# Kernel tuning notes

Measured on AMD Instinct MI355X. Metric: run time of the kernel, lower is better.

The kernel has to match this reference:

```python
import jax, jax.numpy as jnp
import numpy as np

B, H, W, C = 32, 512, 512, 3


def setup_inputs() -> dict:
    key = jax.random.key(0)
    k1, k2, k3 = jax.random.split(key, 3)
    images = jax.random.normal(k1, (B, H, W, C), dtype=jnp.float32)
    # focal lengths in pixels, positive and well-conditioned
    focal = 400.0 + 200.0 * jax.random.uniform(k2, (B, 2), dtype=jnp.float32)
    # quaternion ~ identity rotation + small noise (stddev=0.01), q0 mean 1
    q = jnp.array([1.0, 0.0, 0.0, 0.0], jnp.float32) + 0.01 * jax.random.normal(k3, (4,), dtype=jnp.float32)
    return {"images": images, "focal": focal, "q": q}


def _quaternion_to_R(q):
    # matches tf_quaternion_to_R: normalize so sum(q^2)=2, then outer product
    q = q * jnp.sqrt(2.0 / jnp.sum(q * q))
    Q = q[:, None] * q[None, :]  # [4,4], Q[i,j] = q_i q_j
    return jnp.array([
        [1.0 - Q[2, 2] - Q[3, 3], Q[1, 2] - Q[3, 0], Q[1, 3] + Q[2, 0]],
        [Q[1, 2] + Q[3, 0], 1.0 - Q[1, 1] - Q[3, 3], Q[2, 3] - Q[1, 0]],
        [Q[1, 3] - Q[2, 0], Q[2, 3] + Q[1, 0], 1.0 - Q[1, 1] - Q[2, 2]],
    ])


def _forward(images, focal, q):
    R = _quaternion_to_R(q)  # [3,3]
    d = jnp.concatenate([focal, jnp.ones((focal.shape[0], 1), focal.dtype)], axis=1)  # [B,3]
    # H = K @ R @ inv(K) with K = diag(d):  H[b,i,j] = d[b,i] * R[i,j] / d[b,j]
    Hm = R[None, :, :] * d[:, :, None] / d[:, None, :]  # [B,3,3]

    origin_x = jnp.float32(W / 2)
    origin_y = jnp.float32(H / 2)
    xs = jnp.arange(W, dtype=jnp.float32) - origin_x  # [W]
    ys = jnp.arange(H, dtype=jnp.float32) - origin_y  # [H]
    x, y = jnp.meshgrid(xs, ys)  # [H,W] each
    ps = jnp.stack([x.ravel(), y.ravel(), jnp.ones(H * W, jnp.float32)], axis=0)  # [3,N]

    ps_w = jnp.einsum('bij,jn->bin', Hm, ps)  # [B,3,N]
    x_w = (ps_w[:, 0, :] / ps_w[:, 2, :]).reshape(-1, H, W) + origin_x  # [B,H,W]
    y_w = (ps_w[:, 1, :] / ps_w[:, 2, :]).reshape(-1, H, W) + origin_y  # [B,H,W]

    # bilinear resampler (tf.contrib.resampler): zero outside image bounds
    x0 = jnp.floor(x_w)
    y0 = jnp.floor(y_w)
    wx = x_w - x0
    wy = y_w - y0
    x0i = x0.astype(jnp.int32)
    y0i = y0.astype(jnp.int32)

    b = jnp.arange(images.shape[0])[:, None, None]

    def corner(yi, xi, w):
        valid = (xi >= 0) & (xi <= W - 1) & (yi >= 0) & (yi <= H - 1)
        g = images[b, jnp.clip(yi, 0, H - 1), jnp.clip(xi, 0, W - 1)]  # [B,H,W,C]
        return g * (w * valid.astype(images.dtype))[..., None]

    out = (corner(y0i, x0i, (1.0 - wx) * (1.0 - wy))
           + corner(y0i, x0i + 1, wx * (1.0 - wy))
           + corner(y0i + 1, x0i, (1.0 - wx) * wy)
           + corner(y0i + 1, x0i + 1, wx * wy))
    return out


def reference(images, focal, q):
    return _forward(images, focal, q)
```

## Files before the change

### kernel.cpp

```cpp
#include <hip/hip_runtime.h>
#include <hip/hip_bf16.h>


#define IMG_H 512
#define IMG_W 512
#define IMG_C 3
#define NB    32

typedef float f32x4u __attribute__((ext_vector_type(4), aligned(4)));
typedef float f32x2u __attribute__((ext_vector_type(2), aligned(4)));

__global__ __launch_bounds__(256) void warp_kernel(
    const float* __restrict__ images,
    const float* __restrict__ focal,
    const float* __restrict__ q,
    float* __restrict__ out)
{
    const unsigned bid  = blockIdx.x;
    const unsigned xcd  = bid & 7u;
    const unsigned slot = bid >> 3;
    const unsigned virt = xcd * 2048u + slot;
    const int b = (int)(virt >> 9);
    const int y = (int)(virt & 511u);

    const int tid = threadIdx.x;

    float q0 = q[0], q1 = q[1], q2 = q[2], q3 = q[3];
    {
        float s = sqrtf(2.0f / (q0*q0 + q1*q1 + q2*q2 + q3*q3));
        q0 *= s; q1 *= s; q2 *= s; q3 *= s;
    }
    const float R00 = 1.0f - q2*q2 - q3*q3;
    const float R01 = q1*q2 - q3*q0;
    const float R02 = q1*q3 + q2*q0;
    const float R10 = q1*q2 + q3*q0;
    const float R11 = 1.0f - q1*q1 - q3*q3;
    const float R12 = q2*q3 - q1*q0;
    const float R20 = q1*q3 - q2*q0;
    const float R21 = q2*q3 + q1*q0;
    const float R22 = 1.0f - q1*q1 - q2*q2;
    const float d0 = focal[b*2 + 0];
    const float d1 = focal[b*2 + 1];

    const float h0 = (R00*d0)/d0;
    const float h1 = (R01*d0)/d1;
    const float h2 = (R02*d0);
    const float h3 = (R10*d1)/d0;
    const float h4 = (R11*d1)/d1;
    const float h5 = (R12*d1);
    const float h6 = R20/d0;
    const float h7 = R21/d1;
    const float h8 = R22;

    const float ys = (float)y - 256.0f;
    const float r1 = h1*ys + h2;
    const float r4 = h4*ys + h5;
    const float r7 = h7*ys + h8;

    const float* __restrict__ img_b = images + (unsigned)b * (IMG_H * IMG_W * IMG_C);

    #define SAMPLE(PX, A0, A1, A2) do {                                        \
        const float xs = (float)(PX) - 256.0f;                                 \
        float p0 = fmaf(h0, xs, r1);                                           \
        float p1 = fmaf(h3, xs, r4);                                           \
        float p2 = fmaf(h6, xs, r7);                                           \
        float rp2 = __builtin_amdgcn_rcpf(p2);                                 \
        float xw = fmaf(p0, rp2, 256.0f);                                      \
        float yw = fmaf(p1, rp2, 256.0f);                                      \
        float x0f = floorf(xw), y0f = floorf(yw);                              \
        float wx = xw - x0f,   wy = yw - y0f;                                  \
        int x0 = (int)x0f, y0i = (int)y0f;                                     \
        bool interior = (x0 >= 0) & (y0i >= 0) &                               \
                        (x0 < IMG_W-1) & (y0i < IMG_H-1);                      \
        if (__all(interior)) {                                                 \
             \
            const float* bpA = img_b + ((unsigned)y0i * IMG_W + (unsigned)x0) * 3u; \
            const float* bpB = bpA + IMG_W * 3u;                               \
            f32x4u vA0 = *reinterpret_cast<const f32x4u*>(bpA);                \
            f32x2u vA1 = *reinterpret_cast<const f32x2u*>(bpA + 4);            \
            f32x4u vB0 = *reinterpret_cast<const f32x4u*>(bpB);                \
            f32x2u vB1 = *reinterpret_cast<const f32x2u*>(bpB + 4);            \
            float w00 = (1.0f - wx) * (1.0f - wy);                             \
            float w01 = wx * (1.0f - wy);                                      \
            float w10 = (1.0f - wx) * wy;                                      \
            float w11 = wx * wy;                                               \
            A0 = vA0.x*w00 + vA0.w*w01 + vB0.x*w10 + vB0.w*w11;                \
            A1 = vA0.y*w00 + vA1.x*w01 + vB0.y*w10 + vB1.x*w11;                \
            A2 = vA0.z*w00 + vA1.y*w01 + vB0.z*w10 + vB1.y*w11;                \
        } else {                                                               \
                          \
            int x1 = x0 + 1, y1i = y0i + 1;                                    \
            bool vx0 = (x0 >= 0) & (x0 <= IMG_W-1);                            \
            bool vx1 = (x1 >= 0) & (x1 <= IMG_W-1);                            \
            bool vy0 = (y0i >= 0) & (y0i <= IMG_H-1);                          \
            bool vy1 = (y1i >= 0) & (y1i <= IMG_H-1);                          \
            unsigned xc0 = (unsigned)min(max(x0, 0), IMG_W-1);                 \
            unsigned xc1 = (unsigned)min(max(x1, 0), IMG_W-1);                 \
            unsigned yc0 = (unsigned)min(max(y0i, 0), IMG_H-1);                \
            unsigned yc1 = (unsigned)min(max(y1i, 0), IMG_H-1);                \
            const float* p00 = img_b + (yc0 * IMG_W + xc0) * IMG_C;            \
            const float* p01 = img_b + (yc0 * IMG_W + xc1) * IMG_C;            \
            const float* p10 = img_b + (yc1 * IMG_W + xc0) * IMG_C;            \
            const float* p11 = img_b + (yc1 * IMG_W + xc1) * IMG_C;            \
            float a00 = p00[0], a01 = p00[1], a02 = p00[2];                    \
            float b00 = p01[0], b01 = p01[1], b02 = p01[2];                    \
            float c00 = p10[0], c01 = p10[1], c02 = p10[2];                    \
            float d00 = p11[0], d01 = p11[1], d02 = p11[2];                    \
            float w00 = (vx0 & vy0) ? (1.0f - wx) * (1.0f - wy) : 0.0f;        \
            float w01 = (vx1 & vy0) ? wx * (1.0f - wy)          : 0.0f;        \
            float w10 = (vx0 & vy1) ? (1.0f - wx) * wy          : 0.0f;        \
            float w11 = (vx1 & vy1) ? wx * wy                   : 0.0f;        \
            A0 = a00*w00 + b00*w01 + c00*w10 + d00*w11;                        \
            A1 = a01*w00 + b01*w01 + c01*w10 + d01*w11;                        \
            A2 = a02*w00 + b02*w01 + c02*w10 + d02*w11;                        \
        }                                                                      \
    } while (0)

    const int px = tid * 2;
    float o0a, o1a, o2a, o0b, o1b, o2b;
    SAMPLE(px,     o0a, o1a, o2a);
    SAMPLE(px + 1, o0b, o1b, o2b);
    #undef SAMPLE

    float* outp = out + ((unsigned)(b * IMG_H + y)) * (IMG_W * IMG_C) + (unsigned)px * 3u;
    f32x4u s0; s0.x = o0a; s0.y = o1a; s0.z = o2a; s0.w = o0b;
    f32x2u s1; s1.x = o1b; s1.y = o2b;
    __builtin_nontemporal_store(s0, reinterpret_cast<f32x4u*>(outp));
    __builtin_nontemporal_store(s1, reinterpret_cast<f32x2u*>(outp + 4));
}

extern "C" void kernel_launch(void* const* d_in, const int* in_sizes, int n_in,
                              void* d_out, int out_size, void* d_ws, size_t ws_size,
                              hipStream_t stream) {
    const float* images = (const float*)d_in[0];
    const float* focal  = (const float*)d_in[1];
    const float* q      = (const float*)d_in[2];
    float* out = (float*)d_out;

    dim3 grid(16384);
    dim3 block(256);
    warp_kernel<<<grid, block, 0, stream>>>(images, focal, q, out);
}
```

Measured before the change: 38.92 us.

## Process eight rows per block with LDS-staged coalesced output stores

Each block now handles eight consecutive output rows instead of one, and the grid shrinks accordingly so per-block setup (quaternion, homography) is amortized. Each thread samples strided pixels tid and tid+256, and the results are staged in a double-buffered shared-memory row so global stores are aligned 16-byte coalesced vectors. This adds a __syncthreads per row and LDS traffic, and the strided pixel assignment changes the gather access pattern relative to the previous adjacent-pair scheme.

```diff
diff --git a/kernel.cpp b/kernel.cpp
--- a/kernel.cpp
+++ b/kernel.cpp
@@ -7,6 +7,7 @@
 #define IMG_C 3
 #define NB    32
 
+typedef float f32x4  __attribute__((ext_vector_type(4)));
 typedef float f32x4u __attribute__((ext_vector_type(4), aligned(4)));
 typedef float f32x2u __attribute__((ext_vector_type(2), aligned(4)));
 
@@ -19,11 +20,13 @@
     const unsigned bid  = blockIdx.x;
     const unsigned xcd  = bid & 7u;
     const unsigned slot = bid >> 3;
-    const unsigned virt = xcd * 2048u + slot;
-    const int b = (int)(virt >> 9);
-    const int y = (int)(virt & 511u);
+    const unsigned virt = xcd * 256u + slot;
+    const int b  = (int)(virt >> 6);
+    const int yg = (int)(virt & 63u) * 8;
 
     const int tid = threadIdx.x;
+
+    __shared__ float s_out[2][IMG_W * IMG_C];
 
     float q0 = q[0], q1 = q[1], q2 = q[2], q3 = q[3];
     {
@@ -52,18 +55,13 @@
     const float h7 = R21/d1;
     const float h8 = R22;
 
-    const float ys = (float)y - 256.0f;
-    const float r1 = h1*ys + h2;
-    const float r4 = h4*ys + h5;
-    const float r7 = h7*ys + h8;
-
     const float* __restrict__ img_b = images + (unsigned)b * (IMG_H * IMG_W * IMG_C);
 
-    #define SAMPLE(PX, A0, A1, A2) do {                                        \
+    #define SAMPLE(PX, R1, R4, R7, A0, A1, A2) do {                            \
         const float xs = (float)(PX) - 256.0f;                                 \
-        float p0 = fmaf(h0, xs, r1);                                           \
-        float p1 = fmaf(h3, xs, r4);                                           \
-        float p2 = fmaf(h6, xs, r7);                                           \
+        float p0 = fmaf(h0, xs, R1);                                           \
+        float p1 = fmaf(h3, xs, R4);                                           \
+        float p2 = fmaf(h6, xs, R7);                                           \
         float rp2 = __builtin_amdgcn_rcpf(p2);                                 \
         float xw = fmaf(p0, rp2, 256.0f);                                      \
         float yw = fmaf(p1, rp2, 256.0f);                                      \
@@ -116,17 +114,37 @@
         }                                                                      \
     } while (0)
 
-    const int px = tid * 2;
-    float o0a, o1a, o2a, o0b, o1b, o2b;
-    SAMPLE(px,     o0a, o1a, o2a);
-    SAMPLE(px + 1, o0b, o1b, o2b);
+    #pragma unroll 2
+    for (int i = 0; i < 8; ++i) {
+        const int y = yg + i;
+        const float ys = (float)y - 256.0f;
+        const float r1 = fmaf(h1, ys, h2);
+        const float r4 = fmaf(h4, ys, h5);
+        const float r7 = fmaf(h7, ys, h8);
+
+        float o0a, o1a, o2a, o0b, o1b, o2b;
+        SAMPLE(tid,       r1, r4, r7, o0a, o1a, o2a);
+        SAMPLE(tid + 256, r1, r4, r7, o0b, o1b, o2b);
+
+        float* buf = s_out[i & 1];
+        buf[tid*3 + 0] = o0a;
+        buf[tid*3 + 1] = o1a;
+        buf[tid*3 + 2] = o2a;
+        buf[(tid + 256)*3 + 0] = o0b;
+        buf[(tid + 256)*3 + 1] = o1b;
+        buf[(tid + 256)*3 + 2] = o2b;
+        __syncthreads();
+
+        f32x4* outp = reinterpret_cast<f32x4*>(
+            out + ((unsigned)(b * IMG_H + y)) * (IMG_W * IMG_C));
+        f32x4 v0 = *reinterpret_cast<const f32x4*>(&buf[tid * 4]);
+        __builtin_nontemporal_store(v0, &outp[tid]);
+        if (tid < 128) {
+            f32x4 v1 = *reinterpret_cast<const f32x4*>(&buf[(256 + tid) * 4]);
+            __builtin_nontemporal_store(v1, &outp[256 + tid]);
+        }
+    }
     #undef SAMPLE
-
-    float* outp = out + ((unsigned)(b * IMG_H + y)) * (IMG_W * IMG_C) + (unsigned)px * 3u;
-    f32x4u s0; s0.x = o0a; s0.y = o1a; s0.z = o2a; s0.w = o0b;
-    f32x2u s1; s1.x = o1b; s1.y = o2b;
-    __builtin_nontemporal_store(s0, reinterpret_cast<f32x4u*>(outp));
-    __builtin_nontemporal_store(s1, reinterpret_cast<f32x2u*>(outp + 4));
 }
 
 extern "C" void kernel_launch(void* const* d_in, const int* in_sizes, int n_in,
@@ -137,7 +155,7 @@
     const float* q      = (const float*)d_in[2];
     float* out = (float*)d_out;
 
-    dim3 grid(16384);
+    dim3 grid(2048);
     dim3 block(256);
     warp_kernel<<<grid, block, 0, stream>>>(images, focal, q, out);
 }
```

New measurement: 39.42 us. Within noise of the previous version (+1.3%).

## Share gather loads between adjacent pixels and stage output through LDS

Applied to the files above, without the earlier changes.

When both pixels of a thread fall in the same source row and their x-offsets differ by 0 or 1, a single set of wider loads from the two source rows serves both bilinear samples. This replaces two separate gathers per pixel. Results are written to shared memory first and then stored as aligned 16-byte vectors, so the global writes are fully coalesced instead of unaligned 4+2-float stores. The cost is a block-wide barrier, 6KB of LDS per block and extra select logic for the paired path.

```diff
diff --git a/kernel.cpp b/kernel.cpp
--- a/kernel.cpp
+++ b/kernel.cpp
@@ -7,8 +7,8 @@
 #define IMG_C 3
 #define NB    32
 
+typedef float f32x4  __attribute__((ext_vector_type(4)));
 typedef float f32x4u __attribute__((ext_vector_type(4), aligned(4)));
-typedef float f32x2u __attribute__((ext_vector_type(2), aligned(4)));
 
 __global__ __launch_bounds__(256) void warp_kernel(
     const float* __restrict__ images,
@@ -24,6 +24,8 @@
     const int y = (int)(virt & 511u);
 
     const int tid = threadIdx.x;
+
+    __shared__ float s_out[IMG_W * IMG_C];
 
     float q0 = q[0], q1 = q[1], q2 = q[2], q3 = q[3];
     {
@@ -59,44 +61,88 @@
 
     const float* __restrict__ img_b = images + (unsigned)b * (IMG_H * IMG_W * IMG_C);
 
-    #define SAMPLE(PX, A0, A1, A2) do {                                        \
-        const float xs = (float)(PX) - 256.0f;                                 \
-        float p0 = fmaf(h0, xs, r1);                                           \
-        float p1 = fmaf(h3, xs, r4);                                           \
-        float p2 = fmaf(h6, xs, r7);                                           \
-        float rp2 = __builtin_amdgcn_rcpf(p2);                                 \
-        float xw = fmaf(p0, rp2, 256.0f);                                      \
-        float yw = fmaf(p1, rp2, 256.0f);                                      \
-        float x0f = floorf(xw), y0f = floorf(yw);                              \
-        float wx = xw - x0f,   wy = yw - y0f;                                  \
-        int x0 = (int)x0f, y0i = (int)y0f;                                     \
-        bool interior = (x0 >= 0) & (y0i >= 0) &                               \
-                        (x0 < IMG_W-1) & (y0i < IMG_H-1);                      \
-        if (__all(interior)) {                                                 \
-             \
-            const float* bpA = img_b + ((unsigned)y0i * IMG_W + (unsigned)x0) * 3u; \
-            const float* bpB = bpA + IMG_W * 3u;                               \
-            f32x4u vA0 = *reinterpret_cast<const f32x4u*>(bpA);                \
-            f32x2u vA1 = *reinterpret_cast<const f32x2u*>(bpA + 4);            \
-            f32x4u vB0 = *reinterpret_cast<const f32x4u*>(bpB);                \
-            f32x2u vB1 = *reinterpret_cast<const f32x2u*>(bpB + 4);            \
-            float w00 = (1.0f - wx) * (1.0f - wy);                             \
-            float w01 = wx * (1.0f - wy);                                      \
-            float w10 = (1.0f - wx) * wy;                                      \
-            float w11 = wx * wy;                                               \
-            A0 = vA0.x*w00 + vA0.w*w01 + vB0.x*w10 + vB0.w*w11;                \
-            A1 = vA0.y*w00 + vA1.x*w01 + vB0.y*w10 + vB1.x*w11;                \
-            A2 = vA0.z*w00 + vA1.y*w01 + vB0.z*w10 + vB1.y*w11;                \
-        } else {                                                               \
-                          \
-            int x1 = x0 + 1, y1i = y0i + 1;                                    \
-            bool vx0 = (x0 >= 0) & (x0 <= IMG_W-1);                            \
+    const int px = tid * 2;
+    float xwa, ywa, xwb, ywb;
+    {
+        const float xsa = (float)px - 256.0f;
+        float p0 = fmaf(h0, xsa, r1);
+        float p1 = fmaf(h3, xsa, r4);
+        float p2 = fmaf(h6, xsa, r7);
+        float rp = __builtin_amdgcn_rcpf(p2);
+        xwa = fmaf(p0, rp, 256.0f);
+        ywa = fmaf(p1, rp, 256.0f);
+        const float xsb = xsa + 1.0f;
+        float p0b = fmaf(h0, xsb, r1);
+        float p1b = fmaf(h3, xsb, r4);
+        float p2b = fmaf(h6, xsb, r7);
+        float rpb = __builtin_amdgcn_rcpf(p2b);
+        xwb = fmaf(p0b, rpb, 256.0f);
+        ywb = fmaf(p1b, rpb, 256.0f);
+    }
+
+    float x0fa = floorf(xwa), y0fa = floorf(ywa);
+    float x0fb = floorf(xwb), y0fb = floorf(ywb);
+    float wxa = xwa - x0fa, wya = ywa - y0fa;
+    float wxb = xwb - x0fb, wyb = ywb - y0fb;
+    int x0a = (int)x0fa, y0a = (int)y0fa;
+    int x0b = (int)x0fb, y0b = (int)y0fb;
+
+    bool interior_a = (x0a >= 0) & (y0a >= 0) & (x0a < IMG_W-1) & (y0a < IMG_H-1);
+    bool interior_b = (x0b >= 0) & (y0b >= 0) & (x0b < IMG_W-1) & (y0b < IMG_H-1);
+    int  dx = x0b - x0a;
+    bool pairable = interior_a & interior_b & (y0b == y0a) & ((dx == 0) | (dx == 1));
+
+    float o0a, o1a, o2a, o0b, o1b, o2b;
+
+    if (__all(pairable)) {
+        const bool dx1 = (dx == 1);
+        const float* bpA = img_b + ((unsigned)y0a * IMG_W + (unsigned)x0a) * 3u;
+        const float* bpB = bpA + IMG_W * 3u;
+        f32x4u uA0 = *reinterpret_cast<const f32x4u*>(bpA);
+        f32x4u uA1 = *reinterpret_cast<const f32x4u*>(bpA + 4);
+        float  fA8 = *(bpA + (dx1 ? 8 : 0));
+        f32x4u uB0 = *reinterpret_cast<const f32x4u*>(bpB);
+        f32x4u uB1 = *reinterpret_cast<const f32x4u*>(bpB + 4);
+        float  fB8 = *(bpB + (dx1 ? 8 : 0));
+
+        float w00a = (1.0f - wxa) * (1.0f - wya);
+        float w01a = wxa * (1.0f - wya);
+        float w10a = (1.0f - wxa) * wya;
+        float w11a = wxa * wya;
+        o0a = uA0.x*w00a + uA0.w*w01a + uB0.x*w10a + uB0.w*w11a;
+        o1a = uA0.y*w00a + uA1.x*w01a + uB0.y*w10a + uB1.x*w11a;
+        o2a = uA0.z*w00a + uA1.y*w01a + uB0.z*w10a + uB1.y*w11a;
+
+        float c0A0 = dx1 ? uA0.w : uA0.x;
+        float c0A1 = dx1 ? uA1.x : uA0.y;
+        float c0A2 = dx1 ? uA1.y : uA0.z;
+        float c1A0 = dx1 ? uA1.z : uA0.w;
+        float c1A1 = dx1 ? uA1.w : uA1.x;
+        float c1A2 = dx1 ? fA8   : uA1.y;
+        float c0B0 = dx1 ? uB0.w : uB0.x;
+        float c0B1 = dx1 ? uB1.x : uB0.y;
+        float c0B2 = dx1 ? uB1.y : uB0.z;
+        float c1B0 = dx1 ? uB1.z : uB0.w;
+        float c1B1 = dx1 ? uB1.w : uB1.x;
+        float c1B2 = dx1 ? fB8   : uB1.y;
+
+        float w00b = (1.0f - wxb) * (1.0f - wyb);
+        float w01b = wxb * (1.0f - wyb);
+        float w10b = (1.0f - wxb) * wyb;
+        float w11b = wxb * wyb;
+        o0b = c0A0*w00b + c1A0*w01b + c0B0*w10b + c1B0*w11b;
+        o1b = c0A1*w00b + c1A1*w01b + c0B1*w10b + c1B1*w11b;
+        o2b = c0A2*w00b + c1A2*w01b + c0B2*w10b + c1B2*w11b;
+    } else {
+        #define SAMPLE_SLOW(X0, Y0, WX, WY, A0, A1, A2) do {                   \
+            int x1 = (X0) + 1, y1i = (Y0) + 1;                                 \
+            bool vx0 = ((X0) >= 0) & ((X0) <= IMG_W-1);                        \
             bool vx1 = (x1 >= 0) & (x1 <= IMG_W-1);                            \
-            bool vy0 = (y0i >= 0) & (y0i <= IMG_H-1);                          \
+            bool vy0 = ((Y0) >= 0) & ((Y0) <= IMG_H-1);                        \
             bool vy1 = (y1i >= 0) & (y1i <= IMG_H-1);                          \
-            unsigned xc0 = (unsigned)min(max(x0, 0), IMG_W-1);                 \
+            unsigned xc0 = (unsigned)min(max((X0), 0), IMG_W-1);               \
             unsigned xc1 = (unsigned)min(max(x1, 0), IMG_W-1);                 \
-            unsigned yc0 = (unsigned)min(max(y0i, 0), IMG_H-1);                \
+            unsigned yc0 = (unsigned)min(max((Y0), 0), IMG_H-1);               \
             unsigned yc1 = (unsigned)min(max(y1i, 0), IMG_H-1);                \
             const float* p00 = img_b + (yc0 * IMG_W + xc0) * IMG_C;            \
             const float* p01 = img_b + (yc0 * IMG_W + xc1) * IMG_C;            \
@@ -106,27 +152,35 @@
             float b00 = p01[0], b01 = p01[1], b02 = p01[2];                    \
             float c00 = p10[0], c01 = p10[1], c02 = p10[2];                    \
             float d00 = p11[0], d01 = p11[1], d02 = p11[2];                    \
-            float w00 = (vx0 & vy0) ? (1.0f - wx) * (1.0f - wy) : 0.0f;        \
-            float w01 = (vx1 & vy0) ? wx * (1.0f - wy)          : 0.0f;        \
-            float w10 = (vx0 & vy1) ? (1.0f - wx) * wy          : 0.0f;        \
-            float w11 = (vx1 & vy1) ? wx * wy                   : 0.0f;        \
+            float w00 = (vx0 & vy0) ? (1.0f - (WX)) * (1.0f - (WY)) : 0.0f;    \
+            float w01 = (vx1 & vy0) ? (WX) * (1.0f - (WY))          : 0.0f;    \
+            float w10 = (vx0 & vy1) ? (1.0f - (WX)) * (WY)          : 0.0f;    \
+            float w11 = (vx1 & vy1) ? (WX) * (WY)                   : 0.0f;    \
             A0 = a00*w00 + b00*w01 + c00*w10 + d00*w11;                        \
             A1 = a01*w00 + b01*w01 + c01*w10 + d01*w11;                        \
             A2 = a02*w00 + b02*w01 + c02*w10 + d02*w11;                        \
-        }                                                                      \
-    } while (0)
+        } while (0)
+        SAMPLE_SLOW(x0a, y0a, wxa, wya, o0a, o1a, o2a);
+        SAMPLE_SLOW(x0b, y0b, wxb, wyb, o0b, o1b, o2b);
+        #undef SAMPLE_SLOW
+    }
 
-    const int px = tid * 2;
-    float o0a, o1a, o2a, o0b, o1b, o2b;
-    SAMPLE(px,     o0a, o1a, o2a);
-    SAMPLE(px + 1, o0b, o1b, o2b);
-    #undef SAMPLE
+    s_out[px*3 + 0] = o0a;
+    s_out[px*3 + 1] = o1a;
+    s_out[px*3 + 2] = o2a;
+    s_out[px*3 + 3] = o0b;
+    s_out[px*3 + 4] = o1b;
+    s_out[px*3 + 5] = o2b;
+    __syncthreads();
 
-    float* outp = out + ((unsigned)(b * IMG_H + y)) * (IMG_W * IMG_C) + (unsigned)px * 3u;
-    f32x4u s0; s0.x = o0a; s0.y = o1a; s0.z = o2a; s0.w = o0b;
-    f32x2u s1; s1.x = o1b; s1.y = o2b;
-    __builtin_nontemporal_store(s0, reinterpret_cast<f32x4u*>(outp));
-    __builtin_nontemporal_store(s1, reinterpret_cast<f32x2u*>(outp + 4));
+    f32x4* outp = reinterpret_cast<f32x4*>(
+        out + ((unsigned)(b * IMG_H + y)) * (IMG_W * IMG_C));
+    f32x4 v0 = *reinterpret_cast<const f32x4*>(&s_out[tid * 4]);
+    __builtin_nontemporal_store(v0, &outp[tid]);
+    if (tid < 128) {
+        f32x4 v1 = *reinterpret_cast<const f32x4*>(&s_out[(256 + tid) * 4]);
+        __builtin_nontemporal_store(v1, &outp[256 + tid]);
+    }
 }
 
 extern "C" void kernel_launch(void* const* d_in, const int* in_sizes, int n_in,
```

Result: faster. 36.07 us (-7.3%).
